# Kernel optimization log

Hardware: AMD Instinct MI355X
Metric: run time of the kernel (lower is better)

## Reference

```python
import jax, jax.numpy as jnp
import numpy as np

Cl, Nl, Cv, Nv, M = 32, 128, 8, 64, 500000


def _sample1d(line, g):
    # line: [C, N]; g in [-1,1]; align_corners=True, zeros padding
    C, N = line.shape
    ix = (g + 1.0) * 0.5 * (N - 1)
    i0 = jnp.floor(ix)
    w = ix - i0
    i0 = i0.astype(jnp.int32)
    def gth(i, wt):
        valid = (i >= 0) & (i < N)
        return line[:, jnp.clip(i, 0, N - 1)] * (wt * valid)
    return (gth(i0, 1.0 - w) + gth(i0 + 1, w)).T  # [M, C]


def _sample2d(plane, gx, gy):
    # plane: [C, H, W]; grid x -> W axis, y -> H axis (torch grid_sample convention)
    C, H, W = plane.shape
    ix = (gx + 1.0) * 0.5 * (W - 1)
    iy = (gy + 1.0) * 0.5 * (H - 1)
    x0 = jnp.floor(ix); y0 = jnp.floor(iy)
    wx = ix - x0; wy = iy - y0
    x0 = x0.astype(jnp.int32); y0 = y0.astype(jnp.int32)
    flat = plane.reshape(C, -1)
    def gth(xi, yi, wt):
        valid = (xi >= 0) & (xi < W) & (yi >= 0) & (yi < H)
        idx = jnp.clip(yi, 0, H - 1) * W + jnp.clip(xi, 0, W - 1)
        return flat[:, idx] * (wt * valid)
    out = (gth(x0, y0, (1 - wx) * (1 - wy)) + gth(x0 + 1, y0, wx * (1 - wy))
           + gth(x0, y0 + 1, (1 - wx) * wy) + gth(x0 + 1, y0 + 1, wx * wy))
    return out.T  # [M, C]


def _sample3d(vol, gx, gy, gz):
    # vol: [C, D, H, W]; grid (x,y,z) -> (W,H,D) axes
    C, D, H, W = vol.shape
    ix = (gx + 1.0) * 0.5 * (W - 1)
    iy = (gy + 1.0) * 0.5 * (H - 1)
    iz = (gz + 1.0) * 0.5 * (D - 1)
    x0 = jnp.floor(ix); y0 = jnp.floor(iy); z0 = jnp.floor(iz)
    wx = ix - x0; wy = iy - y0; wz = iz - z0
    x0 = x0.astype(jnp.int32); y0 = y0.astype(jnp.int32); z0 = z0.astype(jnp.int32)
    flat = vol.reshape(C, -1)
    out = 0.0
    for dz in (0, 1):
        for dy in (0, 1):
            for dx in (0, 1):
                xi, yi, zi = x0 + dx, y0 + dy, z0 + dz
                wt = ((wx if dx else 1 - wx) * (wy if dy else 1 - wy) * (wz if dz else 1 - wz))
                valid = (xi >= 0) & (xi < W) & (yi >= 0) & (yi < H) & (zi >= 0) & (zi < D)
                idx = (jnp.clip(zi, 0, D - 1) * H + jnp.clip(yi, 0, H - 1)) * W + jnp.clip(xi, 0, W - 1)
                out = out + flat[:, idx] * (wt * valid)
    return out.T  # [M, C]


def setup_inputs() -> dict:
    key = jax.random.key(0)
    ks = jax.random.split(key, 16)
    rng, shift = 0.4, 0.1
    coordinates = jax.random.uniform(ks[0], (1, M, 3), minval=-1.0, maxval=1.0)
    line_x = jax.random.uniform(ks[1], (Cl, Nl)) * rng + shift
    line_y = jax.random.uniform(ks[2], (Cl, Nl)) * rng + shift
    line_z = jax.random.uniform(ks[3], (Cl, Nl)) * rng + shift
    plane_xy = jax.random.normal(ks[4], (Cl, Nl, Nl)) * rng + shift
    plane_yz = jax.random.normal(ks[5], (Cl, Nl, Nl)) * rng + shift
    plane_xz = jax.random.normal(ks[6], (Cl, Nl, Nl)) * rng + shift
    volume = jax.random.normal(ks[7], (Cv, Nv, Nv, Nv)) * rng + shift
    def lin(k, fi, fo):
        k1, k2 = jax.random.split(k)
        lim = 1.0 / np.sqrt(fi)
        return (jax.random.uniform(k1, (fi, fo), minval=-lim, maxval=lim),
                jax.random.uniform(k2, (fo,), minval=-lim, maxval=lim))
    Wx, bx = lin(ks[8], Cl, Cl)
    Wy, by = lin(ks[9], Cl, Cl)
    Wz, bz = lin(ks[10], Cl, Cl)
    W1, b1 = lin(ks[11], Cl + Cv, 128)
    W2, b2 = lin(ks[12], 128, 1)
    return dict(coordinates=coordinates, line_x=line_x, line_y=line_y, line_z=line_z,
                plane_xy=plane_xy, plane_yz=plane_yz, plane_xz=plane_xz, volume=volume,
                Wx=Wx, bx=bx, Wy=Wy, by=by, Wz=Wz, bz=bz, W1=W1, b1=b1, W2=W2, b2=b2)


def reference(coordinates, line_x, line_y, line_z, plane_xy, plane_yz, plane_xz, volume,
              Wx, bx, Wy, by, Wz, bz, W1, b1, W2, b2):
    c = coordinates[0]  # [M, 3], batch squeezed like the torch code
    x, y, z = c[:, 0], c[:, 1], c[:, 2]
    x_e = _sample1d(line_x, x)
    y_e = _sample1d(line_y, y)
    z_e = _sample1d(line_z, z)
    xy_e = _sample2d(plane_xy, x, y)
    yz_e = _sample2d(plane_yz, y, z)
    xz_e = _sample2d(plane_xz, x, z)
    xyz_e = _sample3d(volume, x, y, z)
    phi = lambda e, W, b: jax.nn.relu(e) @ W + b  # Sequential(ReLU, Linear)
    yztran = phi(yz_e, Wx, bx)
    xztran = phi(xz_e, Wy, by)
    xytran = phi(xy_e, Wz, bz)
    xtran = phi(x_e, Wx, bx)
    ytran = phi(y_e, Wy, by)
    ztran = phi(z_e, Wz, bz)
    features = xtran * yztran + ytran * xztran + ztran * xytran
    features = jnp.concatenate([features, xyz_e], axis=-1)  # [M, Cl+Cv]
    h = jax.nn.relu(features @ W1 + b1)
    return h @ W2 + b2  # [M, 1]
```

## Files before the change

### kernel.cpp

```cpp
#include <hip/hip_runtime.h>

typedef unsigned short u16;
typedef u16 u16x8 __attribute__((ext_vector_type(8)));
typedef _Float16 half2 __attribute__((ext_vector_type(2)));
typedef _Float16 h8v __attribute__((ext_vector_type(8)));
typedef float f4v __attribute__((ext_vector_type(4)));

union H8 { h8v v; half2 p[4]; };

static __device__ __forceinline__ float bf2f(u16 u) {
    union { unsigned int i; float f; } v;
    v.i = ((unsigned int)u) << 16;
    return v.f;
}
static __device__ __forceinline__ u16 f2bf(float f) {
    union { float f; unsigned int i; } v;
    v.f = f;
    unsigned int x = v.i;
    x += 0x7fffu + ((x >> 16) & 1u);
    return (u16)(x >> 16);
}
static __device__ __forceinline__ float gld(int dt, const void* p, int i) {
    return dt ? ((const float*)p)[i] : bf2f(((const u16*)p)[i]);
}
static __device__ __forceinline__ int detect_dt(const void* coords) {
    u16 v = ((const u16*)coords)[threadIdx.x & 63];
    int e = (v >> 7) & 0xFF;
    bool inr = (e >= 90) && (e <= 126);
    unsigned long long m = __ballot(inr);
    return (__popcll(m) >= 56) ? 0 : 1;
}
static __device__ __forceinline__ half2 pk(float a, float b) {
    return __builtin_bit_cast(half2, __builtin_amdgcn_cvt_pkrtz(a, b));
}

static __device__ __forceinline__ void lds_wait() {
    asm volatile("s_waitcnt lgkmcnt(0)" ::: "memory");
}

#define WF_OFF        64u
#define PLANES_S_OFF  34304u
#define VOL_S_OFF     3180032u
#define LINES_S_OFF   7374336u
#define WS_NEED       7398912u

static __device__ __forceinline__ void weights_work(
    int dt, int r,
    const void* Wx, const void* bx, const void* Wy, const void* by,
    const void* Wz, const void* bz, const void* W1, const void* b1,
    const void* W2, const void* b2, float* wbase)
{
    _Float16* WtH = (_Float16*)wbase;
    float*    bv  = wbase + 1536;
    _Float16* W1H = (_Float16*)(wbase + 1632);
    float*    b1v = wbase + 5728;
    float*    W2v = wbase + 5856;
    float*    b2v = wbase + 5984;
    if (r < 3072) {
        int m = r >> 10, idx = r & 1023;
        int o = idx >> 5, c = idx & 31;
        const void* s = (m == 0) ? Wx : (m == 1) ? Wy : Wz;
        WtH[r] = (_Float16)gld(dt, s, c * 32 + o);
    } else if (r < 3168) {
        int q2 = r - 3072;
        int m = q2 >> 5, c = q2 & 31;
        const void* s = (m == 0) ? bx : (m == 1) ? by : bz;
        bv[q2] = gld(dt, s, c);
    } else if (r < 11360) {
        int idx = r - 3168;
        int j = idx >> 6, i = idx & 63;
        W1H[idx] = (i < 40) ? (_Float16)gld(dt, W1, i * 128 + j) : (_Float16)0.0f;
    } else if (r < 11488) {
        b1v[r - 11360] = gld(dt, b1, r - 11360);
    } else if (r < 11616) {
        W2v[r - 11488] = gld(dt, W2, r - 11488);
    } else if (r == 11616) {
        b2v[0] = gld(dt, b2, 0);
    }
}

__global__ __launch_bounds__(256) void kp_prep_all(
    const void* __restrict__ coords,
    const void* __restrict__ lx, const void* __restrict__ ly,
    const void* __restrict__ lz,
    const void* __restrict__ pxy, const void* __restrict__ pyz,
    const void* __restrict__ pxz, const void* __restrict__ vol,
    const void* __restrict__ Wx, const void* __restrict__ bx,
    const void* __restrict__ Wy, const void* __restrict__ by,
    const void* __restrict__ Wz, const void* __restrict__ bz,
    const void* __restrict__ W1, const void* __restrict__ b1,
    const void* __restrict__ W2, const void* __restrict__ b2,
    float* __restrict__ wbase,
    u16* __restrict__ planes_s, u16* __restrict__ vol_s,
    u16* __restrict__ lines_s)
{
    int dt = detect_dt(coords);
    int blk = blockIdx.x;
    if (blk < 1798) {
        int t = blk * 256 + threadIdx.x;
        u16x8 v;
        if (t < 196608) {
            int o = t * 8;
            int pl = o >> 19;
            int r  = o & 524287;
            int pos = r >> 5, c0 = r & 31;
            const void* src = (pl == 0) ? pxy : (pl == 1) ? pyz : pxz;
#pragma unroll
            for (int i = 0; i < 8; ++i)
                v[i] = dt ? f2bf(((const float*)src)[(c0 + i) * 16384 + pos])
                          : ((const u16*)src)[(c0 + i) * 16384 + pos];
            *(u16x8*)(planes_s + o) = v;
        } else if (t < 458752) {
            int pos = t - 196608;
#pragma unroll
            for (int c = 0; c < 8; ++c)
                v[c] = dt ? f2bf(((const float*)vol)[c * 262144 + pos])
                          : ((const u16*)vol)[c * 262144 + pos];
            *(u16x8*)(vol_s + pos * 8) = v;
        } else {
            int o = (t - 458752) * 8;
            int l = o >> 12, rr = o & 4095;
            int pos = rr >> 5, c0 = rr & 31;
            const void* src = (l == 0) ? lx : (l == 1) ? ly : lz;
#pragma unroll
            for (int i = 0; i < 8; ++i)
                v[i] = dt ? f2bf(((const float*)src)[(c0 + i) * 128 + pos])
                          : ((const u16*)src)[(c0 + i) * 128 + pos];
            *(u16x8*)(lines_s + o) = v;
        }
    } else {
        int r = (blk - 1798) * 256 + threadIdx.x;
        weights_work(dt, r, Wx, bx, Wy, by, Wz, bz, W1, b1, W2, b2, wbase);
    }
}

struct Samp { int i0, i1; float w0, w1; };

static __device__ __forceinline__ Samp make_samp(float g, int N) {
    float ix = (g + 1.0f) * 0.5f * (float)(N - 1);
    float fl = floorf(ix);
    float w  = ix - fl;
    int i  = (int)fl;
    int i1 = i + 1;
    float v0 = (i  >= 0 && i  < N) ? 1.0f : 0.0f;
    float v1 = (i1 >= 0 && i1 < N) ? 1.0f : 0.0f;
    Samp s;
    s.w0 = (1.0f - w) * v0;
    s.w1 = w * v1;
    s.i0 = min(max(i, 0), N - 1);
    s.i1 = min(max(i1, 0), N - 1);
    return s;
}

#define MFMA16(a, b, c) __builtin_amdgcn_mfma_f32_16x16x32_f16((a), (b), (c), 0, 0, 0)

#define SRE 40
#define SR2 72

struct PL { u16x8 q00[4], q01[4], q10[4], q11[4]; };
struct VL { u16x8 v[8]; };

static __device__ __forceinline__ void plane_load(
    const u16* __restrict__ Ps, const Samp& sa, const Samp& sb, PL& P)
{
    const u16x8* p00 = (const u16x8*)(Ps + (sb.i0 * 128 + sa.i0) * 32);
    const u16x8* p01 = (const u16x8*)(Ps + (sb.i0 * 128 + sa.i1) * 32);
    const u16x8* p10 = (const u16x8*)(Ps + (sb.i1 * 128 + sa.i0) * 32);
    const u16x8* p11 = (const u16x8*)(Ps + (sb.i1 * 128 + sa.i1) * 32);
#pragma unroll
    for (int cc = 0; cc < 4; ++cc) {
        P.q00[cc] = p00[cc]; P.q01[cc] = p01[cc];
        P.q10[cc] = p10[cc]; P.q11[cc] = p11[cc];
    }
}

static __device__ __forceinline__ void vol_loads(
    const u16* __restrict__ vol_s, const Samp& vx, const Samp& vy,
    const Samp& vz, VL& V)
{
#pragma unroll
    for (int corner = 0; corner < 8; ++corner) {
        int dx = corner & 1, dy = (corner >> 1) & 1, dz = corner >> 2;
        int xi = dx ? vx.i1 : vx.i0;
        int yi = dy ? vy.i1 : vy.i0;
        int zi = dz ? vz.i1 : vz.i0;
        V.v[corner] = *(const u16x8*)(vol_s + (((zi * 64) + yi) * 64 + xi) * 8);
    }
}

template<int PRE>
static __device__ __forceinline__ void term_step(
    int lane, int q, int l15,
    const u16* __restrict__ Ls, const Samp& sl,
    const PL& P, const Samp& sa, const Samp& sb,
    const _Float16* __restrict__ Wt, const float* __restrict__ bvt,
    _Float16* El, _Float16* Ep, float (&feat)[4][2][4],
    const u16* __restrict__ nps, const Samp& na, const Samp& nb, PL& PN,
    const u16* __restrict__ vol_s, const Samp& vx, const Samp& vy,
    const Samp& vz, VL& V)
{
    const u16x8* l0 = (const u16x8*)(Ls + sl.i0 * 32);
    const u16x8* l1 = (const u16x8*)(Ls + sl.i1 * 32);
    float w00 = sb.w0 * sa.w0, w01 = sb.w0 * sa.w1;
    float w10 = sb.w1 * sa.w0, w11 = sb.w1 * sa.w1;
#pragma unroll
    for (int cc = 0; cc < 4; ++cc) {
        u16x8 A0 = l0[cc], A1 = l1[cc];
        u16x8 Q00 = P.q00[cc], Q01 = P.q01[cc];
        u16x8 Q10 = P.q10[cc], Q11 = P.q11[cc];
        H8 hl, hp;
#pragma unroll
        for (int kk = 0; kk < 4; ++kk) {
            int k0 = 2 * kk, k1 = k0 + 1;
            float el0 = sl.w0 * bf2f(A0[k0]) + sl.w1 * bf2f(A1[k0]);
            float el1 = sl.w0 * bf2f(A0[k1]) + sl.w1 * bf2f(A1[k1]);
            float ep0 = w00 * bf2f(Q00[k0]) + w01 * bf2f(Q01[k0])
                      + w10 * bf2f(Q10[k0]) + w11 * bf2f(Q11[k0]);
            float ep1 = w00 * bf2f(Q00[k1]) + w01 * bf2f(Q01[k1])
                      + w10 * bf2f(Q10[k1]) + w11 * bf2f(Q11[k1]);
            hl.p[kk] = pk(fmaxf(el0, 0.0f), fmaxf(el1, 0.0f));
            hp.p[kk] = pk(fmaxf(ep0, 0.0f), fmaxf(ep1, 0.0f));
        }
        *(h8v*)&El[lane * SRE + cc * 8] = hl.v;
        *(h8v*)&Ep[lane * SRE + cc * 8] = hp.v;
    }
    if constexpr (PRE == 1) plane_load(nps, na, nb, PN);
    if constexpr (PRE == 2) vol_loads(vol_s, vx, vy, vz, V);

    h8v bf0 = *(const h8v*)&Wt[(l15) * 32 + q * 8];
    h8v bf1 = *(const h8v*)&Wt[(16 + l15) * 32 + q * 8];
    float bb0 = bvt[l15], bb1 = bvt[16 + l15];
    f4v c0 = {bb0, bb0, bb0, bb0};
    f4v c1 = {bb1, bb1, bb1, bb1};
    lds_wait();
#pragma unroll
    for (int mt = 0; mt < 4; ++mt) {
        h8v aL = *(const h8v*)&El[(mt * 16 + l15) * SRE + q * 8];
        h8v aP = *(const h8v*)&Ep[(mt * 16 + l15) * SRE + q * 8];
        f4v ta0 = MFMA16(aL, bf0, c0);
        f4v tb0 = MFMA16(aP, bf0, c0);
        f4v ta1 = MFMA16(aL, bf1, c1);
        f4v tb1 = MFMA16(aP, bf1, c1);
#pragma unroll
        for (int r = 0; r < 4; ++r) {
            feat[mt][0][r] += ta0[r] * tb0[r];
            feat[mt][1][r] += ta1[r] * tb1[r];
        }
    }
    lds_wait();
}

__global__ __launch_bounds__(64) void kp_main_mfma(
    const void* __restrict__ coords,
    const u16* __restrict__ planes_s, const u16* __restrict__ vol_s,
    const u16* __restrict__ lines_s,
    const float* __restrict__ wbase,
    void* __restrict__ out, int M)
{
    __shared__ _Float16 eb[5120];
    __shared__ float res[64];
    int dt = detect_dt(coords);
    const _Float16* WtH = (const _Float16*)wbase;
    const float*    bv  = wbase + 1536;
    const _Float16* W1H = (const _Float16*)(wbase + 1632);
    const float*    b1v = wbase + 5728;
    const float*    W2v = wbase + 5856;
    const float*    b2v = wbase + 5984;

    int lane = threadIdx.x;
    int q = lane >> 4, l15 = lane & 15;
    _Float16* El = eb;
    _Float16* Ep = eb + 2560;
    _Float16* E2 = eb;

    int p = blockIdx.x * 64 + lane;
    p = min(p, M - 1);

    float x, y, z;
    if (dt == 0) {
        const u16* cu = (const u16*)coords;
        x = bf2f(cu[p * 3 + 0]);
        y = bf2f(cu[p * 3 + 1]);
        z = bf2f(cu[p * 3 + 2]);
    } else {
        x = ((const float*)coords)[p * 3 + 0];
        y = ((const float*)coords)[p * 3 + 1];
        z = ((const float*)coords)[p * 3 + 2];
    }

    Samp sx = make_samp(x, 128), sy = make_samp(y, 128), sz = make_samp(z, 128);

    float feat[4][2][4];
#pragma unroll
    for (int mt = 0; mt < 4; ++mt)
#pragma unroll
        for (int n = 0; n < 2; ++n)
#pragma unroll
            for (int r = 0; r < 4; ++r) feat[mt][n][r] = 0.0f;

    PL Pa, Pb;
    VL V;
    Samp vx, vy, vz;

    plane_load(planes_s + 1 * 524288, sy, sz, Pa);

    term_step<1>(lane, q, l15, lines_s + 0 * 4096, sx, Pa, sy, sz,
                 WtH + 0, bv + 0, El, Ep, feat,
                 planes_s + 2 * 524288, sx, sz, Pb,
                 vol_s, sx, sx, sx, V);

    term_step<1>(lane, q, l15, lines_s + 1 * 4096, sy, Pb, sx, sz,
                 WtH + 1024, bv + 32, El, Ep, feat,
                 planes_s + 0 * 524288, sx, sy, Pa,
                 vol_s, sx, sx, sx, V);

    vx = make_samp(x, 64); vy = make_samp(y, 64); vz = make_samp(z, 64);

    term_step<2>(lane, q, l15, lines_s + 2 * 4096, sz, Pa, sx, sy,
                 WtH + 2048, bv + 64, El, Ep, feat,
                 planes_s, sx, sy, Pb,
                 vol_s, vx, vy, vz, V);

#pragma unroll
    for (int mt = 0; mt < 4; ++mt)
#pragma unroll
        for (int n = 0; n < 2; ++n)
#pragma unroll
            for (int r = 0; r < 4; ++r)
                E2[(mt * 16 + q * 4 + r) * SR2 + n * 16 + l15] =
                    (_Float16)feat[mt][n][r];
    {
        float vf[8];
#pragma unroll
        for (int c = 0; c < 8; ++c) vf[c] = 0.0f;
#pragma unroll
        for (int corner = 0; corner < 8; ++corner) {
            int dx = corner & 1, dy = (corner >> 1) & 1, dz = corner >> 2;
            float w = (dx ? vx.w1 : vx.w0) * (dy ? vy.w1 : vy.w0)
                    * (dz ? vz.w1 : vz.w0);
            u16x8 v = V.v[corner];
#pragma unroll
            for (int c = 0; c < 8; ++c)
                vf[c] = fmaf(w, bf2f(v[c]), vf[c]);
        }
        H8 hv;
#pragma unroll
        for (int k = 0; k < 4; ++k) hv.p[k] = pk(vf[2 * k], vf[2 * k + 1]);
        *(h8v*)&E2[lane * SR2 + 32] = hv.v;
        h8v zz = {};
        *(h8v*)&E2[lane * SR2 + 40] = zz;
        *(h8v*)&E2[lane * SR2 + 48] = zz;
        *(h8v*)&E2[lane * SR2 + 56] = zz;
    }
    lds_wait();

    h8v af[4][2];
#pragma unroll
    for (int mt = 0; mt < 4; ++mt)
#pragma unroll
        for (int ks = 0; ks < 2; ++ks)
            af[mt][ks] = *(const h8v*)&E2[(mt * 16 + l15) * SR2 + ks * 32 + q * 8];

    float s[4][4];
#pragma unroll
    for (int mt = 0; mt < 4; ++mt)
#pragma unroll
        for (int r = 0; r < 4; ++r) s[mt][r] = 0.0f;

#pragma unroll
    for (int NT = 0; NT < 8; ++NT) {
        int o = NT * 16 + l15;
        h8v b0  = *(const h8v*)&W1H[o * 64 + q * 8];
        h8v b1f = *(const h8v*)&W1H[o * 64 + 32 + q * 8];
        float w2 = W2v[o];
        float bb = b1v[o];
        f4v cinit = {bb, bb, bb, bb};
#pragma unroll
        for (int mt = 0; mt < 4; ++mt) {
            f4v c = MFMA16(af[mt][0], b0, cinit);
            c = MFMA16(af[mt][1], b1f, c);
#pragma unroll
            for (int r = 0; r < 4; ++r)
                s[mt][r] = fmaf(fmaxf(c[r], 0.0f), w2, s[mt][r]);
        }
    }
#pragma unroll
    for (int mt = 0; mt < 4; ++mt)
#pragma unroll
        for (int r = 0; r < 4; ++r) {
            float v = s[mt][r];
            v += __shfl_xor(v, 1);
            v += __shfl_xor(v, 2);
            v += __shfl_xor(v, 4);
            v += __shfl_xor(v, 8);
            s[mt][r] = v;
        }
    if (l15 == 0) {
#pragma unroll
        for (int mt = 0; mt < 4; ++mt)
#pragma unroll
            for (int r = 0; r < 4; ++r)
                res[mt * 16 + q * 4 + r] = s[mt][r];
    }
    lds_wait();
    float rr = res[lane] + b2v[0];
    if (dt) ((float*)out)[p] = rr;
    else    ((u16*)out)[p]   = f2bf(rr);
}

__global__ void kp_prep_weights_fb(
    const void* __restrict__ coords,
    const void* __restrict__ Wx, const void* __restrict__ bx,
    const void* __restrict__ Wy, const void* __restrict__ by,
    const void* __restrict__ Wz, const void* __restrict__ bz,
    const void* __restrict__ W1, const void* __restrict__ b1,
    const void* __restrict__ W2, const void* __restrict__ b2,
    float* __restrict__ wbase)
{
    int dt = detect_dt(coords);
    int t = blockIdx.x * blockDim.x + threadIdx.x;
    weights_work(dt, t, Wx, bx, Wy, by, Wz, bz, W1, b1, W2, b2, wbase);
}

__global__ __launch_bounds__(256) void kp_main_direct(
    const void* __restrict__ coords,
    const void* __restrict__ lx, const void* __restrict__ ly, const void* __restrict__ lz,
    const void* __restrict__ pxy, const void* __restrict__ pyz, const void* __restrict__ pxz,
    const void* __restrict__ vol,
    const float* __restrict__ wbase,
    void* __restrict__ out, int M)
{
    int dt = detect_dt(coords);
    const _Float16* WtH = (const _Float16*)wbase;
    const float*    bv  = wbase + 1536;
    const _Float16* W1H = (const _Float16*)(wbase + 1632);
    const float*    b1v = wbase + 5728;
    const float*    W2v = wbase + 5856;
    const float*    b2v = wbase + 5984;

    int p = blockIdx.x * 256 + threadIdx.x;
    p = min(p, M - 1);

    float x = gld(dt, coords, p * 3 + 0);
    float y = gld(dt, coords, p * 3 + 1);
    float z = gld(dt, coords, p * 3 + 2);

    Samp sx = make_samp(x, 128), sy = make_samp(y, 128), sz = make_samp(z, 128);

    float feat[40];
#pragma unroll
    for (int o = 0; o < 40; ++o) feat[o] = 0.0f;

    const void* Ls[3] = {lx, ly, lz};
    const void* Psv[3] = {pyz, pxz, pxy};
    Samp sl3[3] = {sx, sy, sz};
    Samp sa3[3] = {sy, sx, sx};
    Samp sb3[3] = {sz, sz, sy};
#pragma unroll 1
    for (int m = 0; m < 3; ++m) {
        float ta[32], tb[32];
        const float* bvt = bv + m * 32;
        const _Float16* Wt = WtH + m * 1024;
#pragma unroll
        for (int o = 0; o < 32; ++o) { ta[o] = bvt[o]; tb[o] = bvt[o]; }
        Samp sl = sl3[m], sa = sa3[m], sb = sb3[m];
        float w00 = sb.w0 * sa.w0, w01 = sb.w0 * sa.w1;
        float w10 = sb.w1 * sa.w0, w11 = sb.w1 * sa.w1;
        int i00 = sb.i0 * 128 + sa.i0, i01 = sb.i0 * 128 + sa.i1;
        int i10 = sb.i1 * 128 + sa.i0, i11 = sb.i1 * 128 + sa.i1;
#pragma unroll 1
        for (int c = 0; c < 32; ++c) {
            float el = sl.w0 * gld(dt, Ls[m], c * 128 + sl.i0)
                     + sl.w1 * gld(dt, Ls[m], c * 128 + sl.i1);
            float ep = w00 * gld(dt, Psv[m], c * 16384 + i00)
                     + w01 * gld(dt, Psv[m], c * 16384 + i01)
                     + w10 * gld(dt, Psv[m], c * 16384 + i10)
                     + w11 * gld(dt, Psv[m], c * 16384 + i11);
            float r1 = fmaxf(el, 0.0f), r2 = fmaxf(ep, 0.0f);
#pragma unroll
            for (int o = 0; o < 32; ++o) {
                float w = (float)Wt[o * 32 + c];
                ta[o] = fmaf(r1, w, ta[o]);
                tb[o] = fmaf(r2, w, tb[o]);
            }
        }
#pragma unroll
        for (int o = 0; o < 32; ++o) feat[o] = fmaf(ta[o], tb[o], feat[o]);
    }

    Samp vx = make_samp(x, 64), vy = make_samp(y, 64), vz = make_samp(z, 64);
#pragma unroll 1
    for (int corner = 0; corner < 8; ++corner) {
        int dx = corner & 1, dy = (corner >> 1) & 1, dz = corner >> 2;
        int xi = dx ? vx.i1 : vx.i0;
        int yi = dy ? vy.i1 : vy.i0;
        int zi = dz ? vz.i1 : vz.i0;
        float w = (dx ? vx.w1 : vx.w0) * (dy ? vy.w1 : vy.w0) * (dz ? vz.w1 : vz.w0);
        int pos = ((zi * 64) + yi) * 64 + xi;
#pragma unroll
        for (int c = 0; c < 8; ++c)
            feat[32 + c] = fmaf(w, gld(dt, vol, c * 262144 + pos), feat[32 + c]);
    }

    float acc_out = b2v[0];
#pragma unroll 2
    for (int j = 0; j < 128; ++j) {
        float acc = b1v[j];
        const _Float16* wr = W1H + j * 64;
#pragma unroll
        for (int i = 0; i < 40; ++i)
            acc = fmaf(feat[i], (float)wr[i], acc);
        acc_out = fmaf(fmaxf(acc, 0.0f), W2v[j], acc_out);
    }
    if (dt) ((float*)out)[p] = acc_out;
    else    ((u16*)out)[p] = f2bf(acc_out);
}

extern "C" void kernel_launch(void* const* d_in, const int* in_sizes, int n_in,
                              void* d_out, int out_size, void* d_ws, size_t ws_size,
                              hipStream_t stream) {
    const void* coords = d_in[0];
    const void* lx  = d_in[1];
    const void* ly  = d_in[2];
    const void* lz  = d_in[3];
    const void* pxy = d_in[4];
    const void* pyz = d_in[5];
    const void* pxz = d_in[6];
    const void* vol = d_in[7];
    const void* Wx  = d_in[8];
    const void* bx  = d_in[9];
    const void* Wy  = d_in[10];
    const void* by  = d_in[11];
    const void* Wz  = d_in[12];
    const void* bz  = d_in[13];
    const void* W1  = d_in[14];
    const void* b1  = d_in[15];
    const void* W2  = d_in[16];
    const void* b2  = d_in[17];

    int M = in_sizes[0] / 3;

    char* ws = (char*)d_ws;
    float* wbase    = (float*)(ws + WF_OFF);
    u16*   planes_s = (u16*)(ws + PLANES_S_OFF);
    u16*   vol_s    = (u16*)(ws + VOL_S_OFF);
    u16*   lines_s  = (u16*)(ws + LINES_S_OFF);

    if (ws_size >= (size_t)WS_NEED) {
        kp_prep_all<<<1844, 256, 0, stream>>>(coords, lx, ly, lz, pxy, pyz, pxz, vol,
                                              Wx, bx, Wy, by, Wz, bz, W1, b1, W2, b2,
                                              wbase, planes_s, vol_s, lines_s);
        int blocks64 = (M + 63) / 64;
        kp_main_mfma<<<blocks64, 64, 0, stream>>>(coords, planes_s, vol_s, lines_s,
                                                  wbase, d_out, M);
    } else {
        int blocks = (M + 255) / 256;
        kp_prep_weights_fb<<<46, 256, 0, stream>>>(coords, Wx, bx, Wy, by, Wz, bz,
                                                   W1, b1, W2, b2, wbase);
        kp_main_direct<<<blocks, 256, 0, stream>>>(coords, lx, ly, lz, pxy, pyz, pxz,
                                                   vol, wbase, d_out, M);
    }
}
```

Before: 194.3 us.

## Process two point groups per wavefront, prefetching the next group's coordinates and first plane

Each 64-lane block now handles two consecutive groups of 64 points and launches half as many blocks. Loads of the second group's coordinates and its first plane-sample gather are issued inside the first group's epilogue, so their latency overlaps the MLP MFMA work. The cost is higher register pressure from the extra live PL state, and less parallelism from the smaller grid, which may reduce latency hiding across waves.

```diff
diff --git a/kernel.cpp b/kernel.cpp
--- a/kernel.cpp
+++ b/kernel.cpp
@@ -250,6 +250,169 @@
     lds_wait();
 }
 
+template<bool PN>
+static __device__ __forceinline__ void do_point(
+    int dt, int lane, int q, int l15, int p,
+    float x, float y, float z, const PL& Pa0,
+    const void* __restrict__ coords,
+    const u16* __restrict__ planes_s, const u16* __restrict__ vol_s,
+    const u16* __restrict__ lines_s,
+    const _Float16* __restrict__ WtH, const float* __restrict__ bv,
+    const _Float16* __restrict__ W1H, const float* __restrict__ b1v,
+    const float* __restrict__ W2v, const float* __restrict__ b2v,
+    _Float16* El, _Float16* Ep, _Float16* E2, float* res,
+    void* __restrict__ out,
+    int pn, float& xn, float& yn, float& zn, PL& PaN)
+{
+    Samp sx = make_samp(x, 128), sy = make_samp(y, 128), sz = make_samp(z, 128);
+
+    float feat[4][2][4];
+#pragma unroll
+    for (int mt = 0; mt < 4; ++mt)
+#pragma unroll
+        for (int n = 0; n < 2; ++n)
+#pragma unroll
+            for (int r = 0; r < 4; ++r) feat[mt][n][r] = 0.0f;
+
+    PL Pb, Pc;
+    VL V;
+    Samp vx, vy, vz;
+
+    term_step<1>(lane, q, l15, lines_s + 0 * 4096, sx, Pa0, sy, sz,
+                 WtH + 0, bv + 0, El, Ep, feat,
+                 planes_s + 2 * 524288, sx, sz, Pb,
+                 vol_s, sx, sx, sx, V);
+
+    term_step<1>(lane, q, l15, lines_s + 1 * 4096, sy, Pb, sx, sz,
+                 WtH + 1024, bv + 32, El, Ep, feat,
+                 planes_s + 0 * 524288, sx, sy, Pc,
+                 vol_s, sx, sx, sx, V);
+
+    vx = make_samp(x, 64); vy = make_samp(y, 64); vz = make_samp(z, 64);
+
+    term_step<2>(lane, q, l15, lines_s + 2 * 4096, sz, Pc, sx, sy,
+                 WtH + 2048, bv + 64, El, Ep, feat,
+                 planes_s, sx, sy, Pb,
+                 vol_s, vx, vy, vz, V);
+
+    u16 cb0 = 0, cb1 = 0, cb2 = 0;
+    float f0 = 0.f, f1 = 0.f, f2 = 0.f;
+    if constexpr (PN) {
+        if (dt == 0) {
+            const u16* cu = (const u16*)coords;
+            cb0 = cu[pn * 3 + 0];
+            cb1 = cu[pn * 3 + 1];
+            cb2 = cu[pn * 3 + 2];
+        } else {
+            const float* cf = (const float*)coords;
+            f0 = cf[pn * 3 + 0];
+            f1 = cf[pn * 3 + 1];
+            f2 = cf[pn * 3 + 2];
+        }
+    }
+
+#pragma unroll
+    for (int mt = 0; mt < 4; ++mt)
+#pragma unroll
+        for (int n = 0; n < 2; ++n)
+#pragma unroll
+            for (int r = 0; r < 4; ++r)
+                E2[(mt * 16 + q * 4 + r) * SR2 + n * 16 + l15] =
+                    (_Float16)feat[mt][n][r];
+    lds_wait();
+    h8v af0[4];
+    {
+    }
+    {
+        float vf[8];
+#pragma unroll
+        for (int c = 0; c < 8; ++c) vf[c] = 0.0f;
+#pragma unroll
+        for (int corner = 0; corner < 8; ++corner) {
+            int dx = corner & 1, dy = (corner >> 1) & 1, dz = corner >> 2;
+            float w = (dx ? vx.w1 : vx.w0) * (dy ? vy.w1 : vy.w0)
+                    * (dz ? vz.w1 : vz.w0);
+            u16x8 v = V.v[corner];
+#pragma unroll
+            for (int c = 0; c < 8; ++c)
+                vf[c] = fmaf(w, bf2f(v[c]), vf[c]);
+        }
+        H8 hv;
+#pragma unroll
+        for (int k = 0; k < 4; ++k) hv.p[k] = pk(vf[2 * k], vf[2 * k + 1]);
+        *(h8v*)&E2[lane * SR2 + 32] = hv.v;
+        h8v zz = {};
+        *(h8v*)&E2[lane * SR2 + 40] = zz;
+        *(h8v*)&E2[lane * SR2 + 48] = zz;
+        *(h8v*)&E2[lane * SR2 + 56] = zz;
+    }
+    lds_wait();
+
+    h8v af[4][2];
+#pragma unroll
+    for (int mt = 0; mt < 4; ++mt)
+#pragma unroll
+        for (int ks = 0; ks < 2; ++ks)
+            af[mt][ks] = *(const h8v*)&E2[(mt * 16 + l15) * SR2 + ks * 32 + q * 8];
+
+    if constexpr (PN) {
+        if (dt == 0) {
+            xn = bf2f(cb0); yn = bf2f(cb1); zn = bf2f(cb2);
+        } else {
+            xn = f0; yn = f1; zn = f2;
+        }
+        Samp syn = make_samp(yn, 128), szn = make_samp(zn, 128);
+        plane_load(planes_s + 1 * 524288, syn, szn, PaN);
+    }
+
+    float s[4][4];
+#pragma unroll
+    for (int mt = 0; mt < 4; ++mt)
+#pragma unroll
+        for (int r = 0; r < 4; ++r) s[mt][r] = 0.0f;
+
+#pragma unroll
+    for (int NT = 0; NT < 8; ++NT) {
+        int o = NT * 16 + l15;
+        h8v b0  = *(const h8v*)&W1H[o * 64 + q * 8];
+        h8v b1f = *(const h8v*)&W1H[o * 64 + 32 + q * 8];
+        float w2 = W2v[o];
+        float bb = b1v[o];
+        f4v cinit = {bb, bb, bb, bb};
+#pragma unroll
+        for (int mt = 0; mt < 4; ++mt) {
+            f4v c = MFMA16(af[mt][0], b0, cinit);
+            c = MFMA16(af[mt][1], b1f, c);
+#pragma unroll
+            for (int r = 0; r < 4; ++r)
+                s[mt][r] = fmaf(fmaxf(c[r], 0.0f), w2, s[mt][r]);
+        }
+    }
+#pragma unroll
+    for (int mt = 0; mt < 4; ++mt)
+#pragma unroll
+        for (int r = 0; r < 4; ++r) {
+            float v = s[mt][r];
+            v += __shfl_xor(v, 1);
+            v += __shfl_xor(v, 2);
+            v += __shfl_xor(v, 4);
+            v += __shfl_xor(v, 8);
+            s[mt][r] = v;
+        }
+    if (l15 == 0) {
+#pragma unroll
+        for (int mt = 0; mt < 4; ++mt)
+#pragma unroll
+            for (int r = 0; r < 4; ++r)
+                res[mt * 16 + q * 4 + r] = s[mt][r];
+    }
+    lds_wait();
+    float rr = res[lane] + b2v[0];
+    if (dt) ((float*)out)[p] = rr;
+    else    ((u16*)out)[p]   = f2bf(rr);
+    lds_wait();
+}
+
 __global__ __launch_bounds__(64) void kp_main_mfma(
     const void* __restrict__ coords,
     const u16* __restrict__ planes_s, const u16* __restrict__ vol_s,
@@ -273,139 +436,42 @@
     _Float16* Ep = eb + 2560;
     _Float16* E2 = eb;
 
-    int p = blockIdx.x * 64 + lane;
-    p = min(p, M - 1);
-
-    float x, y, z;
+    int base = blockIdx.x * 128;
+    int pA = min(base + lane, M - 1);
+    int pB = min(base + 64 + lane, M - 1);
+
+    float xA, yA, zA;
     if (dt == 0) {
         const u16* cu = (const u16*)coords;
-        x = bf2f(cu[p * 3 + 0]);
-        y = bf2f(cu[p * 3 + 1]);
-        z = bf2f(cu[p * 3 + 2]);
+        xA = bf2f(cu[pA * 3 + 0]);
+        yA = bf2f(cu[pA * 3 + 1]);
+        zA = bf2f(cu[pA * 3 + 2]);
     } else {
-        x = ((const float*)coords)[p * 3 + 0];
-        y = ((const float*)coords)[p * 3 + 1];
-        z = ((const float*)coords)[p * 3 + 2];
-    }
-
-    Samp sx = make_samp(x, 128), sy = make_samp(y, 128), sz = make_samp(z, 128);
-
-    float feat[4][2][4];
-#pragma unroll
-    for (int mt = 0; mt < 4; ++mt)
-#pragma unroll
-        for (int n = 0; n < 2; ++n)
-#pragma unroll
-            for (int r = 0; r < 4; ++r) feat[mt][n][r] = 0.0f;
-
-    PL Pa, Pb;
-    VL V;
-    Samp vx, vy, vz;
-
-    plane_load(planes_s + 1 * 524288, sy, sz, Pa);
-
-    term_step<1>(lane, q, l15, lines_s + 0 * 4096, sx, Pa, sy, sz,
-                 WtH + 0, bv + 0, El, Ep, feat,
-                 planes_s + 2 * 524288, sx, sz, Pb,
-                 vol_s, sx, sx, sx, V);
-
-    term_step<1>(lane, q, l15, lines_s + 1 * 4096, sy, Pb, sx, sz,
-                 WtH + 1024, bv + 32, El, Ep, feat,
-                 planes_s + 0 * 524288, sx, sy, Pa,
-                 vol_s, sx, sx, sx, V);
-
-    vx = make_samp(x, 64); vy = make_samp(y, 64); vz = make_samp(z, 64);
-
-    term_step<2>(lane, q, l15, lines_s + 2 * 4096, sz, Pa, sx, sy,
-                 WtH + 2048, bv + 64, El, Ep, feat,
-                 planes_s, sx, sy, Pb,
-                 vol_s, vx, vy, vz, V);
-
-#pragma unroll
-    for (int mt = 0; mt < 4; ++mt)
-#pragma unroll
-        for (int n = 0; n < 2; ++n)
-#pragma unroll
-            for (int r = 0; r < 4; ++r)
-                E2[(mt * 16 + q * 4 + r) * SR2 + n * 16 + l15] =
-                    (_Float16)feat[mt][n][r];
+        const float* cf = (const float*)coords;
+        xA = cf[pA * 3 + 0];
+        yA = cf[pA * 3 + 1];
+        zA = cf[pA * 3 + 2];
+    }
+    PL PaA;
     {
-        float vf[8];
-#pragma unroll
-        for (int c = 0; c < 8; ++c) vf[c] = 0.0f;
-#pragma unroll
-        for (int corner = 0; corner < 8; ++corner) {
-            int dx = corner & 1, dy = (corner >> 1) & 1, dz = corner >> 2;
-            float w = (dx ? vx.w1 : vx.w0) * (dy ? vy.w1 : vy.w0)
-                    * (dz ? vz.w1 : vz.w0);
-            u16x8 v = V.v[corner];
-#pragma unroll
-            for (int c = 0; c < 8; ++c)
-                vf[c] = fmaf(w, bf2f(v[c]), vf[c]);
-        }
-        H8 hv;
-#pragma unroll
-        for (int k = 0; k < 4; ++k) hv.p[k] = pk(vf[2 * k], vf[2 * k + 1]);
-        *(h8v*)&E2[lane * SR2 + 32] = hv.v;
-        h8v zz = {};
-        *(h8v*)&E2[lane * SR2 + 40] = zz;
-        *(h8v*)&E2[lane * SR2 + 48] = zz;
-        *(h8v*)&E2[lane * SR2 + 56] = zz;
-    }
-    lds_wait();
-
-    h8v af[4][2];
-#pragma unroll
-    for (int mt = 0; mt < 4; ++mt)
-#pragma unroll
-        for (int ks = 0; ks < 2; ++ks)
-            af[mt][ks] = *(const h8v*)&E2[(mt * 16 + l15) * SR2 + ks * 32 + q * 8];
-
-    float s[4][4];
-#pragma unroll
-    for (int mt = 0; mt < 4; ++mt)
-#pragma unroll
-        for (int r = 0; r < 4; ++r) s[mt][r] = 0.0f;
-
-#pragma unroll
-    for (int NT = 0; NT < 8; ++NT) {
-        int o = NT * 16 + l15;
-        h8v b0  = *(const h8v*)&W1H[o * 64 + q * 8];
-        h8v b1f = *(const h8v*)&W1H[o * 64 + 32 + q * 8];
-        float w2 = W2v[o];
-        float bb = b1v[o];
-        f4v cinit = {bb, bb, bb, bb};
-#pragma unroll
-        for (int mt = 0; mt < 4; ++mt) {
-            f4v c = MFMA16(af[mt][0], b0, cinit);
-            c = MFMA16(af[mt][1], b1f, c);
-#pragma unroll
-            for (int r = 0; r < 4; ++r)
-                s[mt][r] = fmaf(fmaxf(c[r], 0.0f), w2, s[mt][r]);
-        }
-    }
-#pragma unroll
-    for (int mt = 0; mt < 4; ++mt)
-#pragma unroll
-        for (int r = 0; r < 4; ++r) {
-            float v = s[mt][r];
-            v += __shfl_xor(v, 1);
-            v += __shfl_xor(v, 2);
-            v += __shfl_xor(v, 4);
-            v += __shfl_xor(v, 8);
-            s[mt][r] = v;
-        }
-    if (l15 == 0) {
-#pragma unroll
-        for (int mt = 0; mt < 4; ++mt)
-#pragma unroll
-            for (int r = 0; r < 4; ++r)
-                res[mt * 16 + q * 4 + r] = s[mt][r];
-    }
-    lds_wait();
-    float rr = res[lane] + b2v[0];
-    if (dt) ((float*)out)[p] = rr;
-    else    ((u16*)out)[p]   = f2bf(rr);
+        Samp syA = make_samp(yA, 128), szA = make_samp(zA, 128);
+        plane_load(planes_s + 1 * 524288, syA, szA, PaA);
+    }
+
+    float xB, yB, zB;
+    PL PaB;
+    do_point<true>(dt, lane, q, l15, pA, xA, yA, zA, PaA,
+                   coords, planes_s, vol_s, lines_s,
+                   WtH, bv, W1H, b1v, W2v, b2v,
+                   El, Ep, E2, res, out,
+                   pB, xB, yB, zB, PaB);
+
+    float xd; PL Pd;
+    do_point<false>(dt, lane, q, l15, pB, xB, yB, zB, PaB,
+                    coords, planes_s, vol_s, lines_s,
+                    WtH, bv, W1H, b1v, W2v, b2v,
+                    El, Ep, E2, res, out,
+                    pB, xd, xd, xd, Pd);
 }
 
 __global__ void kp_prep_weights_fb(
@@ -550,9 +616,9 @@
         kp_prep_all<<<1844, 256, 0, stream>>>(coords, lx, ly, lz, pxy, pyz, pxz, vol,
                                               Wx, bx, Wy, by, Wz, bz, W1, b1, W2, b2,
                                               wbase, planes_s, vol_s, lines_s);
-        int blocks64 = (M + 63) / 64;
-        kp_main_mfma<<<blocks64, 64, 0, stream>>>(coords, planes_s, vol_s, lines_s,
-                                                  wbase, d_out, M);
+        int blocks128 = (M + 127) / 128;
+        kp_main_mfma<<<blocks128, 64, 0, stream>>>(coords, planes_s, vol_s, lines_s,
+                                                   wbase, d_out, M);
     } else {
         int blocks = (M + 255) / 256;
         kp_prep_weights_fb<<<46, 256, 0, stream>>>(coords, Wx, bx, Wy, by, Wz, bz,
```

After: 214.0 us. +10.1%, slower.
